# Optimization experiments

Hardware: AMD Instinct MI355X
Metric: run time of the kernel (lower is better)

## Reference

```python
import jax, jax.numpy as jnp
import numpy as np

R = 12          # resolution (H = W = G); L = R**3 = 1728
HEADS = 12


def setup_inputs() -> dict:
    key = jax.random.key(0)
    k1, k2, k3 = jax.random.split(key, 3)
    B, L, C = 4, R ** 3, 768
    qkv = jax.random.normal(k1, (3, B, L, C), dtype=jnp.float32)
    lepe_w = jax.random.normal(k2, (C, 1, 3, 3, 3), dtype=jnp.float32) * 0.05
    lepe_b = jax.random.normal(k3, (C,), dtype=jnp.float32) * 0.01
    return {"qkv": qkv, "lepe_w": lepe_w, "lepe_b": lepe_b}


def reference(qkv, lepe_w, lepe_b):
    # qkv: [3, B, L, C]; idx=0 => window == full volume, so attention is dense over L.
    q, k, v = qkv[0], qkv[1], qkv[2]
    B, L, C = q.shape
    hd = C // HEADS
    scale = hd ** -0.5

    # im2cswin with full-volume window preserves token order: [B, L, C] -> [B, H, L, d]
    qh = q.reshape(B, L, HEADS, hd).transpose(0, 2, 1, 3)
    kh = k.reshape(B, L, HEADS, hd).transpose(0, 2, 1, 3)

    # get_lepe: v -> [B, C, R, R, R], depthwise 3x3x3 conv (groups=C)
    v_img = v.transpose(0, 2, 1).reshape(B, C, R, R, R)
    lepe = jax.lax.conv_general_dilated(
        v_img, lepe_w, window_strides=(1, 1, 1), padding="SAME",
        dimension_numbers=("NCDHW", "OIDHW", "NCDHW"), feature_group_count=C,
    ) + lepe_b[None, :, None, None, None]
    lepe = lepe.reshape(B, HEADS, hd, L).transpose(0, 1, 3, 2)   # [B, H, L, d]
    vh = v_img.reshape(B, HEADS, hd, L).transpose(0, 1, 3, 2)    # [B, H, L, d]

    attn = jax.nn.softmax(jnp.einsum("bhqd,bhkd->bhqk", qh * scale, kh), axis=-1)
    out = jnp.einsum("bhqk,bhkd->bhqd", attn, vh) + lepe          # [B, H, L, d]

    # windows2img with full window is an inverse reshape back to [B, L, C]
    return out.transpose(0, 2, 1, 3).reshape(B, L, C)
```

## Files before the change

kernel.cpp:

```cpp
#include <hip/hip_runtime.h>

#define RR 12
#define LL 1728
#define CC 768
#define HEADS 12
#define HD 64
#define BATCH 4

typedef __attribute__((ext_vector_type(8))) short bf8;
typedef __attribute__((ext_vector_type(4))) float f4;

__device__ inline unsigned short f2bf(float x) {
  unsigned int u = __float_as_uint(x);
  return (unsigned short)((u + 0x7FFFu + ((u >> 16) & 1u)) >> 16);
}
__device__ inline unsigned short f2bfr(float x) {
  return (unsigned short)((__float_as_uint(x) + 0x8000u) >> 16);
}

__device__ inline float fast_exp2(float x) {
#if __has_builtin(__builtin_amdgcn_exp2f)
  return __builtin_amdgcn_exp2f(x);
#else
  return exp2f(x);
#endif
}

__device__ inline void gld16(const unsigned short* g, unsigned short* l) {
  __builtin_amdgcn_global_load_lds((const __attribute__((address_space(1))) unsigned int*)g,
                                   (__attribute__((address_space(3))) unsigned int*)l, 16, 0, 0);
}

#define QSCALE 0.1803368801111244f

#define NLEPE 5184
#define NPREP 1296

__global__ __launch_bounds__(256) void combined_kernel(const float* __restrict__ qkv,
                                                       const float* __restrict__ w,
                                                       const float* __restrict__ bias,
                                                       unsigned short* __restrict__ qb,
                                                       unsigned short* __restrict__ kb,
                                                       unsigned short* __restrict__ vT,
                                                       float* __restrict__ out) {
  __shared__ __align__(16) unsigned char smem[27648];
  const int bid = blockIdx.x;
  const int t = threadIdx.x;

  if (bid < NLEPE) {
    const int xg = (bid % 3) * 4;
    const int line = (bid / 3) % 144;
    const int ct = (bid / 432) % 3;
    const int b = bid / 1296;
    const int z = line / RR;
    const int y = line % RR;
    const int c0 = ct * 256;
    const int c = c0 + t;
    float* w_lds = (float*)smem;

    {
      const float* wsrc = w + (size_t)c0 * 27;
#pragma unroll
      for (int i = 0; i < 7; ++i) {
        const int idx = i * 256 + t;
        if (idx < 1728) *(float4*)&w_lds[idx * 4] = *(const float4*)&wsrc[idx * 4];
      }
    }
    __syncthreads();
    float wreg[27];
#pragma unroll
    for (int j = 0; j < 27; ++j) wreg[j] = w_lds[t * 27 + j];

    const float* vb = qkv + ((size_t)(2 * BATCH + b)) * LL * CC + c;
    const float bv = bias[c];
    float acc[4] = {bv, bv, bv, bv};

#pragma unroll
    for (int dz = -1; dz <= 1; ++dz) {
#pragma unroll
      for (int dy = -1; dy <= 1; ++dy) {
        const int zz = z + dz, yy = y + dy;
        const bool lineok = ((unsigned)zz < RR) & ((unsigned)yy < RR);
        const int base = (zz * RR + yy) * RR;
        float v6[6];
#pragma unroll
        for (int p = 0; p < 6; ++p) {
          const int xx = xg - 1 + p;
          const bool ok = lineok & ((unsigned)xx < RR);
          const int lp = ok ? base + xx : 0;
          const float vv = vb[(size_t)lp * CC];
          v6[p] = ok ? vv : 0.f;
        }
        const int jb = ((dz + 1) * 3 + (dy + 1)) * 3;
        const float wL = wreg[jb], wC = wreg[jb + 1], wR = wreg[jb + 2];
#pragma unroll
        for (int i = 0; i < 4; ++i)
          acc[i] += wL * v6[i] + wC * v6[i + 1] + wR * v6[i + 2];
      }
    }
    const size_t obase = ((size_t)b * LL + line * RR + xg) * CC + c;
#pragma unroll
    for (int i = 0; i < 4; ++i) out[obase + (size_t)i * CC] = acc[i];

  } else {
    const int p = bid - NLEPE;
    const int lt = p % 27;
    const int h = (p / 27) % HEADS;
    const int b = p / (27 * HEADS);
    unsigned short* tl = (unsigned short*)smem;

    {
      const int r0 = t >> 4;
      const int c4 = (t & 15) * 4;
#pragma unroll
      for (int pi = 0; pi < 4; ++pi) {
        const int row = lt * 64 + pi * 16 + r0;
        const size_t off = ((size_t)b * LL + row) * CC + h * HD + c4;
        const float4 qv = *(const float4*)(qkv + off);
        ushort4 oq;
        oq.x = f2bf(qv.x * QSCALE); oq.y = f2bf(qv.y * QSCALE);
        oq.z = f2bf(qv.z * QSCALE); oq.w = f2bf(qv.w * QSCALE);
        *(ushort4*)(qb + off) = oq;
        const float4 kv = *(const float4*)(qkv + (size_t)BATCH * LL * CC + off);
        ushort4 ok;
        ok.x = f2bf(kv.x); ok.y = f2bf(kv.y); ok.z = f2bf(kv.z); ok.w = f2bf(kv.w);
        *(ushort4*)(kb + off) = ok;
      }
    }

    const float* vsrc = qkv + ((size_t)(2 * BATCH + b)) * LL * CC;
#pragma unroll
    for (int it = 0; it < 4; ++it) {
      const int idx = it * 256 + t;
      const int lrow = idx >> 4;
      const int c4 = (idx & 15) * 4;
      const float4 vv = *(const float4*)(vsrc + (size_t)(lt * 64 + lrow) * CC + h * HD + c4);
      tl[(c4 + 0) * 65 + lrow] = f2bf(vv.x);
      tl[(c4 + 1) * 65 + lrow] = f2bf(vv.y);
      tl[(c4 + 2) * 65 + lrow] = f2bf(vv.z);
      tl[(c4 + 3) * 65 + lrow] = f2bf(vv.w);
    }
    __syncthreads();
#pragma unroll
    for (int it = 0; it < 4; ++it) {
      const int idx = it * 256 + t;
      const int drow = idx >> 4;
      const int u = idx & 15;
      const int s4 = u * 4;
      const int kbase = (((u >> 3) * 2 + (u & 1)) << 4) + (((u >> 1) & 3) << 2);
      ushort4 o;
      o.x = tl[drow * 65 + kbase + 0];
      o.y = tl[drow * 65 + kbase + 1];
      o.z = tl[drow * 65 + kbase + 2];
      o.w = tl[drow * 65 + kbase + 3];
      *(ushort4*)(vT + (((size_t)(b * HEADS + h) * HD + drow) * LL) + lt * 64 + s4) = o;
    }
  }
}

__global__ __launch_bounds__(256) void attn_kernel(const unsigned short* __restrict__ qb,
                                                   const unsigned short* __restrict__ kb,
                                                   const unsigned short* __restrict__ vT,
                                                   float* __restrict__ out) {
  __shared__ unsigned short k_lds[2][64 * 64];
  __shared__ unsigned short v_lds[2][64 * 64];

  const int qt = blockIdx.x;
  const int h = blockIdx.y;
  const int b = blockIdx.z;
  const int t = threadIdx.x;
  const int lane = t & 63;
  const int wave = t >> 6;
  const int m = lane & 15;
  const int quad = lane >> 4;

  bf8 qf[2][2];
#pragma unroll
  for (int sub = 0; sub < 2; ++sub) {
    int row = qt * 128 + sub * 64 + wave * 16 + m;
    row = row < LL ? row : LL - 1;
    const size_t qbase = ((size_t)(b * LL + row)) * CC + h * HD;
    qf[sub][0] = *(const bf8*)(qb + qbase + quad * 8);
    qf[sub][1] = *(const bf8*)(qb + qbase + 32 + quad * 8);
  }

  int koff[2], voff[2], ldsb[2];
#pragma unroll
  for (int j = 0; j < 2; ++j) {
    const int cidx = (j * 4 + wave) * 64 + lane;
    const int row = cidx >> 3;
    const int sc = (cidx & 7) ^ (row & 7);
    koff[j] = row * CC + sc * 8;
    voff[j] = row * LL + sc * 8;
    ldsb[j] = (j * 4 + wave) * 512;
  }

  const unsigned short* kgb = kb + (size_t)b * LL * CC + h * HD;
  const unsigned short* vgb = vT + ((size_t)(b * HEADS + h) * HD) * LL;

  gld16(kgb + koff[0], &k_lds[0][ldsb[0]]);
  gld16(kgb + koff[1], &k_lds[0][ldsb[1]]);
  gld16(vgb + voff[0], &v_lds[0][ldsb[0]]);
  gld16(vgb + voff[1], &v_lds[0][ldsb[1]]);

  f4 o_acc[2][4] = {};
  float psum[2] = {0.f, 0.f};

#define ATTN_BODY(KT, CUR)                                                              \
  {                                                                                     \
    __syncthreads();            \
    if ((KT) < 26) {                                                                    \
      const size_t ko = (size_t)((KT) + 1) * 64 * CC;                                   \
      const int vo = ((KT) + 1) * 64;                                                   \
      gld16(kgb + ko + koff[0], &k_lds[(CUR) ^ 1][ldsb[0]]);                            \
      gld16(kgb + ko + koff[1], &k_lds[(CUR) ^ 1][ldsb[1]]);                            \
      gld16(vgb + vo + voff[0], &v_lds[(CUR) ^ 1][ldsb[0]]);                            \
      gld16(vgb + vo + voff[1], &v_lds[(CUR) ^ 1][ldsb[1]]);                            \
    }                                                                                   \
    f4 s_acc[2][4] = {};                                                                \
    _Pragma("unroll")                                                                   \
    for (int nt = 0; nt < 4; ++nt) {                                                    \
      _Pragma("unroll")                                                                 \
      for (int ks = 0; ks < 2; ++ks) {                                                  \
        const int cc = ((ks * 4 + quad) ^ (m & 7)) * 8;                                 \
        const bf8 kf = *(const bf8*)&k_lds[CUR][(nt * 16 + m) * 64 + cc];               \
        s_acc[0][nt] = __builtin_amdgcn_mfma_f32_16x16x32_bf16(kf, qf[0][ks], s_acc[0][nt], 0, 0, 0); \
        s_acc[1][nt] = __builtin_amdgcn_mfma_f32_16x16x32_bf16(kf, qf[1][ks], s_acc[1][nt], 0, 0, 0); \
      }                                                                                 \
    }                                                                                   \
    bf8 pf[2][2];                                                                       \
    _Pragma("unroll")                                                                   \
    for (int sub = 0; sub < 2; ++sub) {                                                 \
      _Pragma("unroll")                                                                 \
      for (int ks = 0; ks < 2; ++ks) {                                                  \
        union { bf8 v; unsigned int w[4]; } pu;                                         \
        _Pragma("unroll")                                                               \
        for (int bb = 0; bb < 2; ++bb) {                                                \
          const int nt = ks * 2 + bb;                                                   \
          const float p0 = fast_exp2(s_acc[sub][nt][0]);                                \
          const float p1 = fast_exp2(s_acc[sub][nt][1]);                                \
          const float p2 = fast_exp2(s_acc[sub][nt][2]);                                \
          const float p3 = fast_exp2(s_acc[sub][nt][3]);                                \
          psum[sub] += (p0 + p1) + (p2 + p3);                                           \
          pu.w[bb * 2 + 0] = (unsigned int)f2bfr(p0) | ((unsigned int)f2bfr(p1) << 16); \
          pu.w[bb * 2 + 1] = (unsigned int)f2bfr(p2) | ((unsigned int)f2bfr(p3) << 16); \
        }                                                                               \
        pf[sub][ks] = pu.v;                                                             \
      }                                                                                 \
    }                                                                                   \
    _Pragma("unroll")                                                                   \
    for (int nt = 0; nt < 4; ++nt) {                                                    \
      _Pragma("unroll")                                                                 \
      for (int ks = 0; ks < 2; ++ks) {                                                  \
        const int cc = ((ks * 4 + quad) ^ (m & 7)) * 8;                                 \
        const bf8 vf = *(const bf8*)&v_lds[CUR][(nt * 16 + m) * 64 + cc];               \
        o_acc[0][nt] = __builtin_amdgcn_mfma_f32_16x16x32_bf16(vf, pf[0][ks], o_acc[0][nt], 0, 0, 0); \
        o_acc[1][nt] = __builtin_amdgcn_mfma_f32_16x16x32_bf16(vf, pf[1][ks], o_acc[1][nt], 0, 0, 0); \
      }                                                                                 \
    }                                                                                   \
  }

  for (int ktp = 0; ktp < 13; ++ktp) {
    const int kt0 = ktp * 2;
    ATTN_BODY(kt0, 0)
    ATTN_BODY(kt0 + 1, 1)
  }
  ATTN_BODY(26, 0)
#undef ATTN_BODY

#pragma unroll
  for (int sub = 0; sub < 2; ++sub) {
    float s = psum[sub];
    s += __shfl_xor(s, 16);
    s += __shfl_xor(s, 32);
    const float inv = 1.0f / s;
    const int rowq = qt * 128 + sub * 64 + wave * 16 + m;
    if (rowq < LL) {
      float* op = out + ((size_t)b * LL + rowq) * CC + h * HD + quad * 4;
#pragma unroll
      for (int nt = 0; nt < 4; ++nt) {
        float4 o4 = *(float4*)&op[nt * 16];
        o4.x += o_acc[sub][nt][0] * inv;
        o4.y += o_acc[sub][nt][1] * inv;
        o4.z += o_acc[sub][nt][2] * inv;
        o4.w += o_acc[sub][nt][3] * inv;
        *(float4*)&op[nt * 16] = o4;
      }
    }
  }
}

extern "C" void kernel_launch(void* const* d_in, const int* in_sizes, int n_in,
                              void* d_out, int out_size, void* d_ws, size_t ws_size,
                              hipStream_t stream) {
  (void)in_sizes; (void)n_in; (void)ws_size; (void)out_size;
  const float* qkv = (const float*)d_in[0];
  const float* lepe_w = (const float*)d_in[1];
  const float* lepe_b = (const float*)d_in[2];
  float* out = (float*)d_out;

  const size_t NE = (size_t)BATCH * LL * CC;
  unsigned short* qb = (unsigned short*)d_ws;
  unsigned short* kb = qb + NE;
  unsigned short* vT = kb + NE;

  combined_kernel<<<dim3(NLEPE + NPREP), 256, 0, stream>>>(qkv, lepe_w, lepe_b, qb, kb, vT, out);
  attn_kernel<<<dim3(14, HEADS, BATCH), 256, 0, stream>>>(qb, kb, vT, out);
}
```

Measured before the change: 191.4 us.

## Triple-buffer K/V tiles with explicit vmcnt waits, XCD-aware block mapping, and setprio

Moves the attention K/V staging from double to triple buffering, so two tiles are in flight while one is computed. Each step waits with an explicit vmcnt count and a raw barrier instead of a full __syncthreads. The grid is flattened to 1D and remapped so the blocks of a given (batch, head) land on the same XCD, which is meant to improve L2 reuse of K/V. s_setprio is raised around the MFMA sections. LDS use grows by half, and correctness depends on the manual waitcnt values matching the number of outstanding loads.

```diff
diff --git a/kernel.cpp b/kernel.cpp
--- a/kernel.cpp
+++ b/kernel.cpp
@@ -162,12 +162,17 @@
                                                    const unsigned short* __restrict__ kb,
                                                    const unsigned short* __restrict__ vT,
                                                    float* __restrict__ out) {
-  __shared__ unsigned short k_lds[2][64 * 64];
-  __shared__ unsigned short v_lds[2][64 * 64];
-
-  const int qt = blockIdx.x;
-  const int h = blockIdx.y;
-  const int b = blockIdx.z;
+  __shared__ unsigned short k_lds[3][64 * 64];
+  __shared__ unsigned short v_lds[3][64 * 64];
+
+  const int g = blockIdx.x;
+  const int xcd = g & 7;
+  const int ix = g >> 3;
+  const int qt = ix % 14;
+  const int bh = xcd * 6 + ix / 14;
+  const int h = bh % HEADS;
+  const int b = bh / HEADS;
+
   const int t = threadIdx.x;
   const int lane = t & 63;
   const int wave = t >> 6;
@@ -198,26 +203,29 @@
   const unsigned short* kgb = kb + (size_t)b * LL * CC + h * HD;
   const unsigned short* vgb = vT + ((size_t)(b * HEADS + h) * HD) * LL;
 
-  gld16(kgb + koff[0], &k_lds[0][ldsb[0]]);
-  gld16(kgb + koff[1], &k_lds[0][ldsb[1]]);
-  gld16(vgb + voff[0], &v_lds[0][ldsb[0]]);
-  gld16(vgb + voff[1], &v_lds[0][ldsb[1]]);
+#define ISSUE_TILE(KT, BUF)                                                             \
+  {                                                                                     \
+    const size_t ko = (size_t)(KT) * 64 * CC;                                           \
+    const int vo = (KT) * 64;                                                           \
+    gld16(kgb + ko + koff[0], &k_lds[BUF][ldsb[0]]);                                    \
+    gld16(kgb + ko + koff[1], &k_lds[BUF][ldsb[1]]);                                    \
+    gld16(vgb + vo + voff[0], &v_lds[BUF][ldsb[0]]);                                    \
+    gld16(vgb + vo + voff[1], &v_lds[BUF][ldsb[1]]);                                    \
+  }
+
+  ISSUE_TILE(0, 0)
+  ISSUE_TILE(1, 1)
 
   f4 o_acc[2][4] = {};
   float psum[2] = {0.f, 0.f};
 
-#define ATTN_BODY(KT, CUR)                                                              \
+#define ATTN_BODY(KT, CUR, WAITN, DOISSUE)                                              \
   {                                                                                     \
-    __syncthreads();            \
-    if ((KT) < 26) {                                                                    \
-      const size_t ko = (size_t)((KT) + 1) * 64 * CC;                                   \
-      const int vo = ((KT) + 1) * 64;                                                   \
-      gld16(kgb + ko + koff[0], &k_lds[(CUR) ^ 1][ldsb[0]]);                            \
-      gld16(kgb + ko + koff[1], &k_lds[(CUR) ^ 1][ldsb[1]]);                            \
-      gld16(vgb + vo + voff[0], &v_lds[(CUR) ^ 1][ldsb[0]]);                            \
-      gld16(vgb + vo + voff[1], &v_lds[(CUR) ^ 1][ldsb[1]]);                            \
-    }                                                                                   \
+    __asm__ volatile("s_waitcnt vmcnt(" #WAITN ")" ::: "memory");                       \
+    __builtin_amdgcn_s_barrier();                                                       \
+    if (DOISSUE) ISSUE_TILE((KT) + 2, ((CUR) + 2) % 3)                                  \
     f4 s_acc[2][4] = {};                                                                \
+    __builtin_amdgcn_s_setprio(1);                                                      \
     _Pragma("unroll")                                                                   \
     for (int nt = 0; nt < 4; ++nt) {                                                    \
       _Pragma("unroll")                                                                 \
@@ -228,6 +236,7 @@
         s_acc[1][nt] = __builtin_amdgcn_mfma_f32_16x16x32_bf16(kf, qf[1][ks], s_acc[1][nt], 0, 0, 0); \
       }                                                                                 \
     }                                                                                   \
+    __builtin_amdgcn_s_setprio(0);                                                      \
     bf8 pf[2][2];                                                                       \
     _Pragma("unroll")                                                                   \
     for (int sub = 0; sub < 2; ++sub) {                                                 \
@@ -248,6 +257,7 @@
         pf[sub][ks] = pu.v;                                                             \
       }                                                                                 \
     }                                                                                   \
+    __builtin_amdgcn_s_setprio(1);                                                      \
     _Pragma("unroll")                                                                   \
     for (int nt = 0; nt < 4; ++nt) {                                                    \
       _Pragma("unroll")                                                                 \
@@ -258,15 +268,20 @@
         o_acc[1][nt] = __builtin_amdgcn_mfma_f32_16x16x32_bf16(vf, pf[1][ks], o_acc[1][nt], 0, 0, 0); \
       }                                                                                 \
     }                                                                                   \
-  }
-
-  for (int ktp = 0; ktp < 13; ++ktp) {
-    const int kt0 = ktp * 2;
-    ATTN_BODY(kt0, 0)
-    ATTN_BODY(kt0 + 1, 1)
-  }
-  ATTN_BODY(26, 0)
+    __builtin_amdgcn_s_setprio(0);                                                      \
+  }
+
+  for (int i = 0; i < 8; ++i) {
+    const int t0 = i * 3;
+    ATTN_BODY(t0 + 0, 0, 4, true)
+    ATTN_BODY(t0 + 1, 1, 4, true)
+    ATTN_BODY(t0 + 2, 2, 4, true)
+  }
+  ATTN_BODY(24, 0, 4, true)
+  ATTN_BODY(25, 1, 4, false)
+  ATTN_BODY(26, 2, 0, false)
 #undef ATTN_BODY
+#undef ISSUE_TILE
 
 #pragma unroll
   for (int sub = 0; sub < 2; ++sub) {
@@ -305,5 +320,5 @@
   unsigned short* vT = kb + NE;
 
   combined_kernel<<<dim3(NLEPE + NPREP), 256, 0, stream>>>(qkv, lepe_w, lepe_b, qb, kb, vT, out);
-  attn_kernel<<<dim3(14, HEADS, BATCH), 256, 0, stream>>>(qb, kb, vT, out);
-}
+  attn_kernel<<<dim3(672), 256, 0, stream>>>(qb, kb, vT, out);
+}
```

Result: no change. 189.5 us (-1.0%).
